# Kernel tuning notes

Measured on AMD Instinct MI355X. Metric: run time of the kernel, lower is better.

## Reference

```python
import jax, jax.numpy as jnp
import numpy as np


def setup_inputs() -> dict:
    key = jax.random.key(0)
    kx, ky = jax.random.split(key)
    B, N, D = 16, 2048, 3
    x = jax.random.normal(kx, (B, N, D), dtype=jnp.float32)
    y = jax.random.normal(ky, (B, N, D), dtype=jnp.float32)
    return {"x": x, "y": y}


def reference(x, y):
    # Squared norms: same math as diag(bmm(x, x^T)) but O(N*D) instead of O(N^2*D).
    rx = jnp.sum(x * x, axis=-1)  # [B, N] -> |x_i|^2
    ry = jnp.sum(y * y, axis=-1)  # [B, N] -> |y_j|^2
    zz = jnp.einsum('bnd,bmd->bnm', x, y)  # [B, N, N] Gram cross term
    # P[b, i, j] = |x_i|^2 + |y_j|^2 - 2 x_i . y_j  (squared Euclidean distance)
    P = rx[:, :, None] + ry[:, None, :] - 2.0 * zz
    dl = jnp.min(P, axis=1)  # min over i: for each y_j, nearest x  -> [B, N]
    dr = jnp.min(P, axis=2)  # min over j: for each x_i, nearest y  -> [B, N]
    cd_loss = jnp.mean(dl, axis=1) + jnp.mean(dr, axis=1)  # [B]
    return cd_loss
```

## Files before the change

kernel.cpp:

```cpp
#include <hip/hip_runtime.h>
#include <float.h>


constexpr int B_ = 16;
constexpr int N_ = 2048;
constexpr int THREADS = 256;
constexpr int QPT = 8;
constexpr int QP2 = QPT / 2;
constexpr int SLICES = N_ / THREADS;

typedef float v2f __attribute__((ext_vector_type(2)));


template <int NJC>
__global__ __launch_bounds__(THREADS)
void cd_min_kernel(const float* __restrict__ x,
                   const float* __restrict__ y,
                   float* __restrict__ partial) {
    constexpr int CHUNK = N_ / NJC;
    const int jc  = blockIdx.x;
    const int b   = blockIdx.y;
    const int dir = blockIdx.z;

    const float* __restrict__ q = dir ? y : x;
    const float* __restrict__ r = dir ? x : y;

    __shared__ float lref[4][CHUNK];
    {
        const float* __restrict__ rp =
            r + ((size_t)b * N_ + (size_t)jc * CHUNK) * 3;
        for (int p = (int)threadIdx.x; p < CHUNK; p += THREADS) {
            const float rx = rp[3 * p + 0];
            const float ry = rp[3 * p + 1];
            const float rz = rp[3 * p + 2];
            lref[0][p] = rx;
            lref[1][p] = ry;
            lref[2][p] = rz;
            lref[3][p] = 0.5f * (rx * rx + ry * ry + rz * rz);
        }
    }

    const int i0 = (int)threadIdx.x * QPT;
    const float* qp = q + ((size_t)b * N_ + i0) * 3;

    v2f nqx[QP2], nqy[QP2], nqz[QP2], q2[QP2], best[QP2];
    #pragma unroll
    for (int k = 0; k < QP2; ++k) {
        const float a0 = qp[6 * k + 0], a1 = qp[6 * k + 1], a2 = qp[6 * k + 2];
        const float b0 = qp[6 * k + 3], b1 = qp[6 * k + 4], b2 = qp[6 * k + 5];
        nqx[k] = (v2f){-a0, -b0};
        nqy[k] = (v2f){-a1, -b1};
        nqz[k] = (v2f){-a2, -b2};
        q2[k]  = (v2f){a0 * a0 + a1 * a1 + a2 * a2,
                       b0 * b0 + b1 * b1 + b2 * b2};
        best[k] = (v2f){FLT_MAX, FLT_MAX};
    }
    __syncthreads();

    const v2f* __restrict__ lx = (const v2f*)lref[0];
    const v2f* __restrict__ ly = (const v2f*)lref[1];
    const v2f* __restrict__ lz = (const v2f*)lref[2];
    const v2f* __restrict__ lh = (const v2f*)lref[3];

    #pragma unroll 4
    for (int j2 = 0; j2 < CHUNK / 2; ++j2) {
        const v2f sx = lx[j2], sy = ly[j2], sz = lz[j2], sh = lh[j2];
        const v2f X0 = (v2f){sx.x, sx.x}, X1 = (v2f){sx.y, sx.y};
        const v2f Y0 = (v2f){sy.x, sy.x}, Y1 = (v2f){sy.y, sy.y};
        const v2f Z0 = (v2f){sz.x, sz.x}, Z1 = (v2f){sz.y, sz.y};
        const v2f H0 = (v2f){sh.x, sh.x}, H1 = (v2f){sh.y, sh.y};
        #pragma unroll
        for (int k = 0; k < QP2; ++k) {
            v2f a = __builtin_elementwise_fma(nqx[k], X0, H0);
            a = __builtin_elementwise_fma(nqy[k], Y0, a);
            a = __builtin_elementwise_fma(nqz[k], Z0, a);
            v2f c = __builtin_elementwise_fma(nqx[k], X1, H1);
            c = __builtin_elementwise_fma(nqy[k], Y1, c);
            c = __builtin_elementwise_fma(nqz[k], Z1, c);
            best[k] = __builtin_elementwise_min(
                best[k], __builtin_elementwise_min(a, c));
        }
    }

    float res[QPT];
    #pragma unroll
    for (int k = 0; k < QP2; ++k) {
        res[2 * k + 0] = 2.0f * best[k].x + q2[k].x;
        res[2 * k + 1] = 2.0f * best[k].y + q2[k].y;
    }
    float4* op = (float4*)(partial
        + (((size_t)dir * B_ + b) * NJC + jc) * N_ + i0);
    op[0] = *(float4*)&res[0];
    op[1] = *(float4*)&res[4];
}

template <int NJC>
__global__ __launch_bounds__(THREADS)
void cd_combine_kernel(const float* __restrict__ partial,
                       float* __restrict__ sums) {
    const int b     = blockIdx.x;
    const int dir   = blockIdx.y;
    const int slice = blockIdx.z;
    const int t     = (int)threadIdx.x;
    const int i     = slice * THREADS + t;

    const float* __restrict__ p =
        partial + ((size_t)dir * B_ + b) * (size_t)NJC * N_ + i;

    float m = FLT_MAX;
    #pragma unroll
    for (int c = 0; c < NJC; ++c)
        m = fminf(m, p[(size_t)c * N_]);

    float s = m;
    #pragma unroll
    for (int o = 32; o > 0; o >>= 1)
        s += __shfl_down(s, o, 64);

    __shared__ float red[THREADS / 64];
    if ((t & 63) == 0) red[t >> 6] = s;
    __syncthreads();
    if (t == 0) {
        float tot = 0.0f;
        #pragma unroll
        for (int w = 0; w < THREADS / 64; ++w) tot += red[w];
        sums[((size_t)dir * B_ + b) * SLICES + slice] = tot;
    }
}

__global__ __launch_bounds__(THREADS)
void cd_final_kernel(const float* __restrict__ sums,
                     float* __restrict__ out) {
    const int t   = (int)threadIdx.x;
    const int b   = t >> 4;
    const int k   = t & 15;
    const int dir = k >> 3;
    const int sl  = k & 7;

    float v = sums[((size_t)dir * B_ + b) * SLICES + sl];
    v += __shfl_down(v, 8, 16);
    v += __shfl_down(v, 4, 16);
    v += __shfl_down(v, 2, 16);
    v += __shfl_down(v, 1, 16);
    if (k == 0) out[b] = v * (1.0f / (float)N_);
}

extern "C" void kernel_launch(void* const* d_in, const int* in_sizes, int n_in,
                              void* d_out, int out_size, void* d_ws, size_t ws_size,
                              hipStream_t stream) {
    const float* x = (const float*)d_in[0];
    const float* y = (const float*)d_in[1];
    float* out     = (float*)d_out;
    float* partial = (float*)d_ws;

    auto need = [](int njc) -> size_t {
        return 2ull * B_ * njc * N_ * sizeof(float)
             + 2ull * B_ * SLICES * sizeof(float);
    };

    const dim3 gcomb(B_, 2, SLICES);
    if (ws_size >= need(32)) {
        float* sums = partial + 2ull * B_ * 32 * N_;
        cd_min_kernel<32><<<dim3(32, B_, 2), dim3(THREADS), 0, stream>>>(x, y, partial);
        cd_combine_kernel<32><<<gcomb, dim3(THREADS), 0, stream>>>(partial, sums);
        cd_final_kernel<<<dim3(1), dim3(THREADS), 0, stream>>>(sums, out);
    } else if (ws_size >= need(16)) {
        float* sums = partial + 2ull * B_ * 16 * N_;
        cd_min_kernel<16><<<dim3(16, B_, 2), dim3(THREADS), 0, stream>>>(x, y, partial);
        cd_combine_kernel<16><<<gcomb, dim3(THREADS), 0, stream>>>(partial, sums);
        cd_final_kernel<<<dim3(1), dim3(THREADS), 0, stream>>>(sums, out);
    } else {
        float* sums = partial + 2ull * B_ * 8 * N_;
        cd_min_kernel<8><<<dim3(8, B_, 2), dim3(THREADS), 0, stream>>>(x, y, partial);
        cd_combine_kernel<8><<<gcomb, dim3(THREADS), 0, stream>>>(partial, sums);
        cd_final_kernel<<<dim3(1), dim3(THREADS), 0, stream>>>(sums, out);
    }
}
```

Measured before the change: 24.61 us.

## Halve queries per thread, split queries across blocks, vectorize over reference pairs

Each thread now handles 4 query points instead of 8, and the query range is split into two slices across extra blocks, doubling the grid. The inner loop packs two reference points per v2f lane instead of two queries, so the scalar broadcast shuffles are gone. launch_bounds asks for 8 blocks per CU. More blocks mean more reference loads into shared memory and less register reuse per LDS read, traded for higher occupancy and parallelism.

```diff
diff --git a/kernel.cpp b/kernel.cpp
--- a/kernel.cpp
+++ b/kernel.cpp
@@ -5,20 +5,22 @@
 constexpr int B_ = 16;
 constexpr int N_ = 2048;
 constexpr int THREADS = 256;
-constexpr int QPT = 8;
-constexpr int QP2 = QPT / 2;
+constexpr int QPT = 4;
+constexpr int QBLK = THREADS * QPT;
+constexpr int QSLICES = N_ / QBLK;
 constexpr int SLICES = N_ / THREADS;
 
 typedef float v2f __attribute__((ext_vector_type(2)));
 
 
 template <int NJC>
-__global__ __launch_bounds__(THREADS)
+__global__ __launch_bounds__(THREADS, 8)
 void cd_min_kernel(const float* __restrict__ x,
                    const float* __restrict__ y,
                    float* __restrict__ partial) {
     constexpr int CHUNK = N_ / NJC;
-    const int jc  = blockIdx.x;
+    const int jc  = (int)blockIdx.x % NJC;
+    const int qs  = (int)blockIdx.x / NJC;
     const int b   = blockIdx.y;
     const int dir = blockIdx.z;
 
@@ -40,19 +42,20 @@
         }
     }
 
-    const int i0 = (int)threadIdx.x * QPT;
+    const int i0 = qs * QBLK + (int)threadIdx.x * QPT;
     const float* qp = q + ((size_t)b * N_ + i0) * 3;
 
-    v2f nqx[QP2], nqy[QP2], nqz[QP2], q2[QP2], best[QP2];
+    v2f QX[QPT], QY[QPT], QZ[QPT], best[QPT];
+    float q2[QPT];
     #pragma unroll
-    for (int k = 0; k < QP2; ++k) {
-        const float a0 = qp[6 * k + 0], a1 = qp[6 * k + 1], a2 = qp[6 * k + 2];
-        const float b0 = qp[6 * k + 3], b1 = qp[6 * k + 4], b2 = qp[6 * k + 5];
-        nqx[k] = (v2f){-a0, -b0};
-        nqy[k] = (v2f){-a1, -b1};
-        nqz[k] = (v2f){-a2, -b2};
-        q2[k]  = (v2f){a0 * a0 + a1 * a1 + a2 * a2,
-                       b0 * b0 + b1 * b1 + b2 * b2};
+    for (int k = 0; k < QPT; ++k) {
+        const float a0 = qp[3 * k + 0];
+        const float a1 = qp[3 * k + 1];
+        const float a2 = qp[3 * k + 2];
+        QX[k] = (v2f){-a0, -a0};
+        QY[k] = (v2f){-a1, -a1};
+        QZ[k] = (v2f){-a2, -a2};
+        q2[k] = a0 * a0 + a1 * a1 + a2 * a2;
         best[k] = (v2f){FLT_MAX, FLT_MAX};
     }
     __syncthreads();
@@ -62,21 +65,20 @@
     const v2f* __restrict__ lz = (const v2f*)lref[2];
     const v2f* __restrict__ lh = (const v2f*)lref[3];
 
-    #pragma unroll 4
-    for (int j2 = 0; j2 < CHUNK / 2; ++j2) {
-        const v2f sx = lx[j2], sy = ly[j2], sz = lz[j2], sh = lh[j2];
-        const v2f X0 = (v2f){sx.x, sx.x}, X1 = (v2f){sx.y, sx.y};
-        const v2f Y0 = (v2f){sy.x, sy.x}, Y1 = (v2f){sy.y, sy.y};
-        const v2f Z0 = (v2f){sz.x, sz.x}, Z1 = (v2f){sz.y, sz.y};
-        const v2f H0 = (v2f){sh.x, sh.x}, H1 = (v2f){sh.y, sh.y};
+    #pragma unroll 2
+    for (int j4 = 0; j4 < CHUNK / 4; ++j4) {
+        const v2f sx0 = lx[2 * j4], sx1 = lx[2 * j4 + 1];
+        const v2f sy0 = ly[2 * j4], sy1 = ly[2 * j4 + 1];
+        const v2f sz0 = lz[2 * j4], sz1 = lz[2 * j4 + 1];
+        const v2f sh0 = lh[2 * j4], sh1 = lh[2 * j4 + 1];
         #pragma unroll
-        for (int k = 0; k < QP2; ++k) {
-            v2f a = __builtin_elementwise_fma(nqx[k], X0, H0);
-            a = __builtin_elementwise_fma(nqy[k], Y0, a);
-            a = __builtin_elementwise_fma(nqz[k], Z0, a);
-            v2f c = __builtin_elementwise_fma(nqx[k], X1, H1);
-            c = __builtin_elementwise_fma(nqy[k], Y1, c);
-            c = __builtin_elementwise_fma(nqz[k], Z1, c);
+        for (int k = 0; k < QPT; ++k) {
+            v2f a = __builtin_elementwise_fma(QX[k], sx0, sh0);
+            a = __builtin_elementwise_fma(QY[k], sy0, a);
+            a = __builtin_elementwise_fma(QZ[k], sz0, a);
+            v2f c = __builtin_elementwise_fma(QX[k], sx1, sh1);
+            c = __builtin_elementwise_fma(QY[k], sy1, c);
+            c = __builtin_elementwise_fma(QZ[k], sz1, c);
             best[k] = __builtin_elementwise_min(
                 best[k], __builtin_elementwise_min(a, c));
         }
@@ -84,14 +86,12 @@
 
     float res[QPT];
     #pragma unroll
-    for (int k = 0; k < QP2; ++k) {
-        res[2 * k + 0] = 2.0f * best[k].x + q2[k].x;
-        res[2 * k + 1] = 2.0f * best[k].y + q2[k].y;
-    }
+    for (int k = 0; k < QPT; ++k)
+        res[k] = 2.0f * fminf(best[k].x, best[k].y) + q2[k];
+
     float4* op = (float4*)(partial
         + (((size_t)dir * B_ + b) * NJC + jc) * N_ + i0);
     op[0] = *(float4*)&res[0];
-    op[1] = *(float4*)&res[4];
 }
 
 template <int NJC>
@@ -161,17 +161,17 @@
     const dim3 gcomb(B_, 2, SLICES);
     if (ws_size >= need(32)) {
         float* sums = partial + 2ull * B_ * 32 * N_;
-        cd_min_kernel<32><<<dim3(32, B_, 2), dim3(THREADS), 0, stream>>>(x, y, partial);
+        cd_min_kernel<32><<<dim3(32 * QSLICES, B_, 2), dim3(THREADS), 0, stream>>>(x, y, partial);
         cd_combine_kernel<32><<<gcomb, dim3(THREADS), 0, stream>>>(partial, sums);
         cd_final_kernel<<<dim3(1), dim3(THREADS), 0, stream>>>(sums, out);
     } else if (ws_size >= need(16)) {
         float* sums = partial + 2ull * B_ * 16 * N_;
-        cd_min_kernel<16><<<dim3(16, B_, 2), dim3(THREADS), 0, stream>>>(x, y, partial);
+        cd_min_kernel<16><<<dim3(16 * QSLICES, B_, 2), dim3(THREADS), 0, stream>>>(x, y, partial);
         cd_combine_kernel<16><<<gcomb, dim3(THREADS), 0, stream>>>(partial, sums);
         cd_final_kernel<<<dim3(1), dim3(THREADS), 0, stream>>>(sums, out);
     } else {
         float* sums = partial + 2ull * B_ * 8 * N_;
-        cd_min_kernel<8><<<dim3(8, B_, 2), dim3(THREADS), 0, stream>>>(x, y, partial);
+        cd_min_kernel<8><<<dim3(8 * QSLICES, B_, 2), dim3(THREADS), 0, stream>>>(x, y, partial);
         cd_combine_kernel<8><<<gcomb, dim3(THREADS), 0, stream>>>(partial, sums);
         cd_final_kernel<<<dim3(1), dim3(THREADS), 0, stream>>>(sums, out);
     }
```

Result: slower. 27.70 us (+12.5%).
